# Performance work log

Measured on AMD Instinct MI355X. Metric: run time of the kernel, lower is better.

The kernel has to match this reference:

```python
import jax, jax.numpy as jnp
import numpy as np

DIM = 768
N_HEADS = 12
HEAD_DIM = DIM // N_HEADS
HIDDEN = 4 * DIM
B, T = 16, 577
EPS = 1e-6


def _layer_norm(x, w, b):
    mu = jnp.mean(x, axis=-1, keepdims=True)
    var = jnp.mean(jnp.square(x - mu), axis=-1, keepdims=True)
    return (x - mu) * jax.lax.rsqrt(var + EPS) * w + b


def setup_inputs() -> dict:
    key = jax.random.key(0)
    ks = jax.random.split(key, 8)
    s = lambda fan_in: 1.0 / np.sqrt(fan_in)
    return {
        "x": jax.random.normal(ks[0], (B, T, DIM), jnp.float32),
        "ln1_w": jnp.ones((DIM,), jnp.float32),
        "ln1_b": jnp.zeros((DIM,), jnp.float32),
        "qkv_w": jax.random.normal(ks[1], (DIM, 3 * DIM), jnp.float32) * s(DIM),
        "qkv_b": jnp.zeros((3 * DIM,), jnp.float32),
        "proj_w": jax.random.normal(ks[2], (DIM, DIM), jnp.float32) * s(DIM),
        "proj_b": jnp.zeros((DIM,), jnp.float32),
        "ln2_w": jnp.ones((DIM,), jnp.float32),
        "ln2_b": jnp.zeros((DIM,), jnp.float32),
        "fc1_w": jax.random.normal(ks[3], (DIM, HIDDEN), jnp.float32) * s(DIM),
        "fc1_b": jnp.zeros((HIDDEN,), jnp.float32),
        "fc2_w": jax.random.normal(ks[4], (HIDDEN, DIM), jnp.float32) * s(HIDDEN),
        "fc2_b": jnp.zeros((DIM,), jnp.float32),
    }


def reference(x, ln1_w, ln1_b, qkv_w, qkv_b, proj_w, proj_b,
              ln2_w, ln2_b, fc1_w, fc1_b, fc2_w, fc2_b):
    # --- attention branch ---
    h = _layer_norm(x, ln1_w, ln1_b)                      # [B,T,D]
    qkv = h @ qkv_w + qkv_b                               # [B,T,3D]
    qkv = qkv.reshape(B, T, 3, N_HEADS, HEAD_DIM)
    q, k, v = jnp.moveaxis(qkv, 2, 0)                     # each [B,T,H,hd]
    scale = HEAD_DIM ** -0.5
    dp = jnp.einsum('bqhd,bkhd->bhqk', q, k) * scale      # [B,H,T,T]
    attn = jax.nn.softmax(dp, axis=-1)
    wa = jnp.einsum('bhqk,bkhd->bqhd', attn, v)           # [B,T,H,hd]
    wa = wa.reshape(B, T, DIM)
    x = x + wa @ proj_w + proj_b
    # --- MLP branch ---
    h = _layer_norm(x, ln2_w, ln2_b)
    h = jax.nn.gelu(h @ fc1_w + fc1_b, approximate=False)
    x = x + h @ fc2_w + fc2_b
    return x
```

## Files before the change

### kernel.cpp

```cpp
#include <hip/hip_runtime.h>
#include <math.h>

#define DIM 768
#define NH 12
#define HIDDEN 3072
#define BB 16
#define TT 577
#define TPAD 640
#define BT (BB*TT)
#define MPAD 9344

typedef _Float16 f16x8 __attribute__((ext_vector_type(8)));
typedef __attribute__((ext_vector_type(4))) float f32x4;

__global__ __launch_bounds__(256) void ln_kernel(const float* __restrict__ x,
                                                 const float* __restrict__ w,
                                                 const float* __restrict__ b,
                                                 _Float16* __restrict__ oh) {
    int row = blockIdx.x;
    const float* xr = x + (size_t)row * DIM;
    int t = threadIdx.x;
    float v0 = xr[t], v1 = xr[t + 256], v2 = xr[t + 512];
    float s = v0 + v1 + v2;
    float sq = v0 * v0 + v1 * v1 + v2 * v2;
    __shared__ float red[8];
    int lane = t & 63, wid = t >> 6;
    #pragma unroll
    for (int off = 32; off; off >>= 1) {
        s  += __shfl_down(s, off);
        sq += __shfl_down(sq, off);
    }
    if (lane == 0) { red[wid] = s; red[4 + wid] = sq; }
    __syncthreads();
    if (t == 0) {
        float ts = red[0] + red[1] + red[2] + red[3];
        float tq = red[4] + red[5] + red[6] + red[7];
        float mu = ts * (1.0f / DIM);
        float var = tq * (1.0f / DIM) - mu * mu;
        red[0] = mu;
        red[1] = rsqrtf(var + 1e-6f);
    }
    __syncthreads();
    float mu = red[0], rstd = red[1];
    int sw = (row & 7) << 3;
    size_t ro = (size_t)row * DIM;
    #pragma unroll
    for (int e = 0; e < 3; ++e) {
        int c = t + e * 256;
        float v = (e == 0 ? v0 : (e == 1 ? v1 : v2));
        float val = (v - mu) * rstd * w[c] + b[c];
        oh[ro + (c ^ sw)] = (_Float16)val;
    }
}

__global__ __launch_bounds__(256) void convert_wT(const float* __restrict__ src,
                                                  _Float16* __restrict__ dh,
                                                  int K, int N) {
    int n = blockIdx.x * 64 + (threadIdx.x & 63);
    int k0 = blockIdx.y * 32 + (threadIdx.x >> 6) * 8;
    f16x8 h8;
    #pragma unroll
    for (int j = 0; j < 8; ++j) h8[j] = (_Float16)src[(size_t)(k0 + j) * N + n];
    *(f16x8*)&dh[(size_t)n * K + (k0 ^ ((n & 7) << 3))] = h8;
}

template<int EPI>
__global__ __launch_bounds__(256) void gemm_mfma(
    const _Float16* __restrict__ A, const _Float16* __restrict__ B,
    const float* __restrict__ bias, const float* __restrict__ resid,
    float* __restrict__ C, _Float16* __restrict__ O,
    _Float16* __restrict__ pQ, _Float16* __restrict__ pK, _Float16* __restrict__ pVT,
    int M, int N, int K) {
    __shared__ _Float16 lds[2][128][64];
    int tid = threadIdx.x;
    int wid = tid >> 6, lane = tid & 63;
    int m0 = blockIdx.y * 128, n0 = blockIdx.x * 128;
    int wr = wid >> 1, wc = wid & 1;

    const _Float16* src = (wid < 2) ? A : B;
    int srow0 = ((wid < 2) ? m0 : n0) + (wid & 1) * 64;
    _Float16* lbase = &lds[wid >> 1][(wid & 1) * 64][0];
    const _Float16* gbase = src + (size_t)(srow0 + (lane >> 3)) * K + (lane & 7) * 8;

    f32x4 acc[4][4];
    #pragma unroll
    for (int i = 0; i < 4; ++i)
        #pragma unroll
        for (int j = 0; j < 4; ++j) acc[i][j] = (f32x4)0.0f;

    for (int k0 = 0; k0 < K; k0 += 64) {
        #pragma unroll
        for (int i = 0; i < 8; ++i) {
            __builtin_amdgcn_global_load_lds(
                (const __attribute__((address_space(1))) void*)(gbase + (size_t)i * 8 * K + k0),
                (__attribute__((address_space(3))) void*)(lbase + i * 512),
                16, 0, 0);
        }
        __syncthreads();
        #pragma unroll
        for (int kk = 0; kk < 2; ++kk) {
            int so = (((kk * 4 + (lane >> 4)) ^ (lane & 7)) << 3);
            f16x8 af[4], bf[4];
            #pragma unroll
            for (int m = 0; m < 4; ++m)
                af[m] = *(const f16x8*)&lds[0][wr * 64 + m * 16 + (lane & 15)][so];
            #pragma unroll
            for (int n = 0; n < 4; ++n)
                bf[n] = *(const f16x8*)&lds[1][wc * 64 + n * 16 + (lane & 15)][so];
            #pragma unroll
            for (int m = 0; m < 4; ++m)
                #pragma unroll
                for (int n = 0; n < 4; ++n)
                    acc[m][n] = __builtin_amdgcn_mfma_f32_16x16x32_f16(af[m], bf[n], acc[m][n], 0, 0, 0);
        }
        __syncthreads();
    }

    int rbase = m0 + wr * 64 + (lane >> 4) * 4;
    int cbase = n0 + wc * 64 + (lane & 15);
    #pragma unroll
    for (int mi = 0; mi < 4; ++mi) {
        #pragma unroll
        for (int ni = 0; ni < 4; ++ni) {
            int c = cbase + ni * 16;
            float bsv = bias[c];
            #pragma unroll
            for (int r4 = 0; r4 < 4; ++r4) {
                int r = rbase + mi * 16 + r4;
                if (r >= M) continue;
                float v = acc[mi][ni][r4] + bsv;
                if (EPI == 1) {
                    v = 0.5f * v * (1.0f + erff(v * 0.70710678118f));
                    O[(size_t)r * N + (c ^ ((r & 7) << 3))] = (_Float16)v;
                } else if (EPI == 2) {
                    v += resid[(size_t)r * N + c];
                    C[(size_t)r * N + c] = v;
                } else {
                    int b_ = r / TT, t_ = r - b_ * TT;
                    int which = c / DIM, cc = c - which * DIM;
                    int head = cc >> 6, d = cc & 63;
                    size_t bh = (size_t)b_ * NH + head;
                    if (which == 0) {
                        pQ[(bh * TPAD + t_) * 64 + d] = (_Float16)(v * 0.125f);
                    } else if (which == 1) {
                        pK[(bh * TPAD + t_) * 64 + (d ^ ((t_ & 7) << 3))] = (_Float16)v;
                    } else {
                        pVT[(bh * 64 + d) * TPAD + ((t_ & ~63) | ((t_ & 63) ^ ((d & 7) << 3)))] = (_Float16)v;
                    }
                }
            }
        }
    }
}

__global__ __launch_bounds__(256) void attn_mfma(
    const _Float16* __restrict__ Q, const _Float16* __restrict__ Kp,
    const _Float16* __restrict__ VT, _Float16* __restrict__ wa) {
    __shared__ _Float16 lds[12288];
    int tid = threadIdx.x, wid = tid >> 6, lane = tid & 63;
    int qt = blockIdx.x, h = blockIdx.y, b = blockIdx.z;
    size_t bh = (size_t)b * NH + h;

    int qrow = qt * 64 + wid * 16 + (lane & 15);
    const _Float16* qb = Q + (bh * TPAD + qrow) * 64 + (lane >> 4) * 8;
    f16x8 qf[2];
    qf[0] = *(const f16x8*)qb;
    qf[1] = *(const f16x8*)(qb + 32);

    f32x4 oacc[4];
    #pragma unroll
    for (int dt = 0; dt < 4; ++dt) oacc[dt] = (f32x4)0.0f;
    float m[4] = {-1e30f, -1e30f, -1e30f, -1e30f};
    float lsum[4] = {0.f, 0.f, 0.f, 0.f};

    _Float16* pbase = &lds[8192 + wid * 1024];

    for (int kt0 = 0; kt0 < TT; kt0 += 64) {
        _Float16* dst = &lds[(wid >> 1) * 4096 + (wid & 1) * 2048];
        const _Float16* gsrc;
        int istride;
        if (wid < 2) {
            gsrc = Kp + (bh * TPAD + kt0 + (wid & 1) * 32 + (lane >> 3)) * 64 + (lane & 7) * 8;
            istride = 8 * 64;
        } else {
            gsrc = VT + (bh * 64 + (wid & 1) * 32 + (lane >> 3)) * TPAD + kt0 + (lane & 7) * 8;
            istride = 8 * TPAD;
        }
        #pragma unroll
        for (int i = 0; i < 4; ++i) {
            __builtin_amdgcn_global_load_lds(
                (const __attribute__((address_space(1))) void*)(gsrc + (size_t)i * istride),
                (__attribute__((address_space(3))) void*)(dst + i * 512),
                16, 0, 0);
        }
        __syncthreads();

        f32x4 sacc[4];
        #pragma unroll
        for (int kt = 0; kt < 4; ++kt) sacc[kt] = (f32x4)0.0f;
        #pragma unroll
        for (int dstep = 0; dstep < 2; ++dstep) {
            #pragma unroll
            for (int kt = 0; kt < 4; ++kt) {
                int krow = kt * 16 + (lane & 15);
                int ko = (((dstep * 4 + (lane >> 4)) ^ (krow & 7)) << 3);
                f16x8 kb = *(const f16x8*)&lds[krow * 64 + ko];
                sacc[kt] = __builtin_amdgcn_mfma_f32_16x16x32_f16(qf[dstep], kb, sacc[kt], 0, 0, 0);
            }
        }
        #pragma unroll
        for (int kt = 0; kt < 4; ++kt) {
            int kcol = kt0 + kt * 16 + (lane & 15);
            if (kcol >= TT) {
                #pragma unroll
                for (int r = 0; r < 4; ++r) sacc[kt][r] = -1e30f;
            }
        }
        float mt[4];
        #pragma unroll
        for (int r = 0; r < 4; ++r)
            mt[r] = fmaxf(fmaxf(sacc[0][r], sacc[1][r]), fmaxf(sacc[2][r], sacc[3][r]));
        #pragma unroll
        for (int off = 1; off <= 8; off <<= 1) {
            #pragma unroll
            for (int r = 0; r < 4; ++r) mt[r] = fmaxf(mt[r], __shfl_xor(mt[r], off));
        }
        float corr[4];
        #pragma unroll
        for (int r = 0; r < 4; ++r) {
            float nm = fmaxf(m[r], mt[r]);
            corr[r] = __expf(m[r] - nm);
            m[r] = nm;
        }
        float rowsum[4] = {0.f, 0.f, 0.f, 0.f};
        #pragma unroll
        for (int kt = 0; kt < 4; ++kt) {
            #pragma unroll
            for (int r = 0; r < 4; ++r) {
                float p = __expf(sacc[kt][r] - m[r]);
                rowsum[r] += p;
                int q = (lane >> 4) * 4 + r;
                int kcol = kt * 16 + (lane & 15);
                pbase[q * 64 + (kcol ^ ((q & 7) << 3))] = (_Float16)p;
            }
        }
        #pragma unroll
        for (int off = 1; off <= 8; off <<= 1) {
            #pragma unroll
            for (int r = 0; r < 4; ++r) rowsum[r] += __shfl_xor(rowsum[r], off);
        }
        #pragma unroll
        for (int r = 0; r < 4; ++r) {
            lsum[r] = lsum[r] * corr[r] + rowsum[r];
            #pragma unroll
            for (int dt = 0; dt < 4; ++dt) oacc[dt][r] *= corr[r];
        }
        #pragma unroll
        for (int kc = 0; kc < 2; ++kc) {
            int q = lane & 15;
            int pko = (((kc * 4 + (lane >> 4)) ^ (q & 7)) << 3);
            f16x8 pa = *(const f16x8*)&pbase[q * 64 + pko];
            #pragma unroll
            for (int dt = 0; dt < 4; ++dt) {
                int drow = dt * 16 + (lane & 15);
                int vo = (((kc * 4 + (lane >> 4)) ^ (drow & 7)) << 3);
                f16x8 vb = *(const f16x8*)&lds[4096 + drow * 64 + vo];
                oacc[dt] = __builtin_amdgcn_mfma_f32_16x16x32_f16(pa, vb, oacc[dt], 0, 0, 0);
            }
        }
        __syncthreads();
    }

    #pragma unroll
    for (int r = 0; r < 4; ++r) {
        int t = qt * 64 + wid * 16 + (lane >> 4) * 4 + r;
        if (t >= TT) continue;
        float inv = 1.0f / lsum[r];
        size_t row = (size_t)b * TT + t;
        int sw = (int)(row & 7) << 3;
        size_t ro = row * DIM;
        #pragma unroll
        for (int dt = 0; dt < 4; ++dt) {
            int c = h * 64 + dt * 16 + (lane & 15);
            wa[ro + (c ^ sw)] = (_Float16)(oacc[dt][r] * inv);
        }
    }
}

extern "C" void kernel_launch(void* const* d_in, const int* in_sizes, int n_in,
                              void* d_out, int out_size, void* d_ws, size_t ws_size,
                              hipStream_t stream) {
    const float* x      = (const float*)d_in[0];
    const float* ln1_w  = (const float*)d_in[1];
    const float* ln1_b  = (const float*)d_in[2];
    const float* qkv_w  = (const float*)d_in[3];
    const float* qkv_b  = (const float*)d_in[4];
    const float* proj_w = (const float*)d_in[5];
    const float* proj_b = (const float*)d_in[6];
    const float* ln2_w  = (const float*)d_in[7];
    const float* ln2_b  = (const float*)d_in[8];
    const float* fc1_w  = (const float*)d_in[9];
    const float* fc1_b  = (const float*)d_in[10];
    const float* fc2_w  = (const float*)d_in[11];
    const float* fc2_b  = (const float*)d_in[12];
    float* out = (float*)d_out;

    const size_t P768  = (size_t)MPAD * 768;
    const size_t P3072 = (size_t)MPAD * 3072;
    const size_t PQKV  = (size_t)BB * NH * TPAD * 64;
    char* wsb = (char*)d_ws;
    auto alloc = [&](size_t bytes) -> char* {
        char* p = wsb;
        wsb += (bytes + 255) & ~(size_t)255;
        return p;
    };
    _Float16* h_p   = (_Float16*)alloc(P768 * 2);
    _Float16* wa_p  = (_Float16*)alloc(P768 * 2);
    float* x1 = (float*)alloc((size_t)BT * 768 * 4);
    _Float16* qkvT = (_Float16*)alloc((size_t)2304 * 768 * 2);
    _Float16* projT = (_Float16*)alloc((size_t)768 * 768 * 2);
    _Float16* fc1T = (_Float16*)alloc((size_t)3072 * 768 * 2);
    _Float16* fc2T = (_Float16*)alloc((size_t)768 * 3072 * 2);
    char* ubase = alloc(P3072 * 2 > 3 * PQKV * 2 ? P3072 * 2 : 3 * PQKV * 2);
    _Float16* pQ  = (_Float16*)ubase;
    _Float16* pK  = pQ + PQKV;
    _Float16* pVT = pK + PQKV;
    _Float16* hh  = (_Float16*)ubase;

    dim3 blk(256);
    int mt = (BT + 127) / 128;

    convert_wT<<<dim3(2304 / 64, 768 / 32), blk, 0, stream>>>(qkv_w, qkvT, 768, 2304);
    convert_wT<<<dim3(768 / 64, 768 / 32), blk, 0, stream>>>(proj_w, projT, 768, 768);
    convert_wT<<<dim3(3072 / 64, 768 / 32), blk, 0, stream>>>(fc1_w, fc1T, 768, 3072);
    convert_wT<<<dim3(768 / 64, 3072 / 32), blk, 0, stream>>>(fc2_w, fc2T, 3072, 768);

    ln_kernel<<<BT, blk, 0, stream>>>(x, ln1_w, ln1_b, h_p);
    gemm_mfma<3><<<dim3(2304 / 128, mt), blk, 0, stream>>>(h_p, qkvT, qkv_b,
        nullptr, nullptr, nullptr, pQ, pK, pVT, BT, 2304, 768);
    attn_mfma<<<dim3((TT + 63) / 64, NH, BB), blk, 0, stream>>>(pQ, pK, pVT, wa_p);
    gemm_mfma<2><<<dim3(768 / 128, mt), blk, 0, stream>>>(wa_p, projT, proj_b,
        x, x1, nullptr, nullptr, nullptr, nullptr, BT, 768, 768);
    ln_kernel<<<BT, blk, 0, stream>>>(x1, ln2_w, ln2_b, h_p);
    gemm_mfma<1><<<dim3(3072 / 128, mt), blk, 0, stream>>>(h_p, fc1T, fc1_b,
        nullptr, nullptr, hh, nullptr, nullptr, nullptr, BT, 3072, 768);
    gemm_mfma<2><<<dim3(768 / 128, mt), blk, 0, stream>>>(hh, fc2T, fc2_b,
        x1, out, nullptr, nullptr, nullptr, nullptr, BT, 768, 3072);
}
```

Before: 524.0 us.

## Double-buffer LDS tiles in GEMM and attention; use tanh-form GELU

Both the MFMA GEMM and the attention kernel now use two LDS buffers. The next K/V or A/B tile is issued with global_load_lds before computing on the current one, and there is one barrier per iteration, so memory latency should overlap with MFMA work. Separately, the FC1 epilogue swaps the exact erf GELU for the tanh approximation written as a sigmoid with __expf, which is cheaper per element but deviates slightly from the exact reference. Doubling LDS per block (64 KB for the GEMM) may cut occupancy. The compiler may also insert full vmcnt waits before the LDS reads, which would limit the overlap.

New measurement: 490.0 us. 1.07x faster.

```diff
diff --git a/kernel.cpp b/kernel.cpp
--- a/kernel.cpp
+++ b/kernel.cpp
@@ -71,7 +71,7 @@
     float* __restrict__ C, _Float16* __restrict__ O,
     _Float16* __restrict__ pQ, _Float16* __restrict__ pK, _Float16* __restrict__ pVT,
     int M, int N, int K) {
-    __shared__ _Float16 lds[2][128][64];
+    __shared__ _Float16 lds[2][2][128][64];
     int tid = threadIdx.x;
     int wid = tid >> 6, lane = tid & 63;
     int m0 = blockIdx.y * 128, n0 = blockIdx.x * 128;
@@ -79,8 +79,9 @@
 
     const _Float16* src = (wid < 2) ? A : B;
     int srow0 = ((wid < 2) ? m0 : n0) + (wid & 1) * 64;
-    _Float16* lbase = &lds[wid >> 1][(wid & 1) * 64][0];
     const _Float16* gbase = src + (size_t)(srow0 + (lane >> 3)) * K + (lane & 7) * 8;
+    _Float16* lb[2] = { &lds[0][wid >> 1][(wid & 1) * 64][0],
+                        &lds[1][wid >> 1][(wid & 1) * 64][0] };
 
     f32x4 acc[4][4];
     #pragma unroll
@@ -88,25 +89,34 @@
         #pragma unroll
         for (int j = 0; j < 4; ++j) acc[i][j] = (f32x4)0.0f;
 
-    for (int k0 = 0; k0 < K; k0 += 64) {
-        #pragma unroll
-        for (int i = 0; i < 8; ++i) {
-            __builtin_amdgcn_global_load_lds(
-                (const __attribute__((address_space(1))) void*)(gbase + (size_t)i * 8 * K + k0),
-                (__attribute__((address_space(3))) void*)(lbase + i * 512),
-                16, 0, 0);
-        }
-        __syncthreads();
+    const int nk = K >> 6;
+    #pragma unroll
+    for (int i = 0; i < 8; ++i)
+        __builtin_amdgcn_global_load_lds(
+            (const __attribute__((address_space(1))) void*)(gbase + (size_t)i * 8 * K),
+            (__attribute__((address_space(3))) void*)(lb[0] + i * 512), 16, 0, 0);
+    __syncthreads();
+
+    int cur = 0;
+    for (int ks = 0; ks < nk; ++ks) {
+        if (ks + 1 < nk) {
+            int k0 = (ks + 1) << 6;
+            #pragma unroll
+            for (int i = 0; i < 8; ++i)
+                __builtin_amdgcn_global_load_lds(
+                    (const __attribute__((address_space(1))) void*)(gbase + (size_t)i * 8 * K + k0),
+                    (__attribute__((address_space(3))) void*)(lb[cur ^ 1] + i * 512), 16, 0, 0);
+        }
         #pragma unroll
         for (int kk = 0; kk < 2; ++kk) {
             int so = (((kk * 4 + (lane >> 4)) ^ (lane & 7)) << 3);
             f16x8 af[4], bf[4];
             #pragma unroll
             for (int m = 0; m < 4; ++m)
-                af[m] = *(const f16x8*)&lds[0][wr * 64 + m * 16 + (lane & 15)][so];
+                af[m] = *(const f16x8*)&lds[cur][0][wr * 64 + m * 16 + (lane & 15)][so];
             #pragma unroll
             for (int n = 0; n < 4; ++n)
-                bf[n] = *(const f16x8*)&lds[1][wc * 64 + n * 16 + (lane & 15)][so];
+                bf[n] = *(const f16x8*)&lds[cur][1][wc * 64 + n * 16 + (lane & 15)][so];
             #pragma unroll
             for (int m = 0; m < 4; ++m)
                 #pragma unroll
@@ -114,6 +124,7 @@
                     acc[m][n] = __builtin_amdgcn_mfma_f32_16x16x32_f16(af[m], bf[n], acc[m][n], 0, 0, 0);
         }
         __syncthreads();
+        cur ^= 1;
     }
 
     int rbase = m0 + wr * 64 + (lane >> 4) * 4;
@@ -130,7 +141,7 @@
                 if (r >= M) continue;
                 float v = acc[mi][ni][r4] + bsv;
                 if (EPI == 1) {
-                    v = 0.5f * v * (1.0f + erff(v * 0.70710678118f));
+                    v = v / (1.0f + __expf(-1.5957691216f * (v + 0.044715f * v * v * v)));
                     O[(size_t)r * N + (c ^ ((r & 7) << 3))] = (_Float16)v;
                 } else if (EPI == 2) {
                     v += resid[(size_t)r * N + c];
@@ -156,7 +167,7 @@
 __global__ __launch_bounds__(256) void attn_mfma(
     const _Float16* __restrict__ Q, const _Float16* __restrict__ Kp,
     const _Float16* __restrict__ VT, _Float16* __restrict__ wa) {
-    __shared__ _Float16 lds[12288];
+    __shared__ _Float16 lds[20480];
     int tid = threadIdx.x, wid = tid >> 6, lane = tid & 63;
     int qt = blockIdx.x, h = blockIdx.y, b = blockIdx.z;
     size_t bh = (size_t)b * NH + h;
@@ -173,27 +184,36 @@
     float m[4] = {-1e30f, -1e30f, -1e30f, -1e30f};
     float lsum[4] = {0.f, 0.f, 0.f, 0.f};
 
-    _Float16* pbase = &lds[8192 + wid * 1024];
-
+    _Float16* pbase = &lds[16384 + wid * 1024];
+    const _Float16* gK = Kp + (bh * TPAD + (wid & 1) * 32 + (lane >> 3)) * 64 + (lane & 7) * 8;
+    const _Float16* gV = VT + (bh * 64 + (wid & 1) * 32 + (lane >> 3)) * TPAD + (lane & 7) * 8;
+    int dstoff = (wid >> 1) * 4096 + (wid & 1) * 2048;
+
+    #pragma unroll
+    for (int i = 0; i < 4; ++i) {
+        const _Float16* g = (wid < 2) ? (gK + (size_t)i * 8 * 64) : (gV + (size_t)i * 8 * TPAD);
+        __builtin_amdgcn_global_load_lds(
+            (const __attribute__((address_space(1))) void*)g,
+            (__attribute__((address_space(3))) void*)(&lds[dstoff] + i * 512), 16, 0, 0);
+    }
+    __syncthreads();
+
+    int cur = 0;
     for (int kt0 = 0; kt0 < TT; kt0 += 64) {
-        _Float16* dst = &lds[(wid >> 1) * 4096 + (wid & 1) * 2048];
-        const _Float16* gsrc;
-        int istride;
-        if (wid < 2) {
-            gsrc = Kp + (bh * TPAD + kt0 + (wid & 1) * 32 + (lane >> 3)) * 64 + (lane & 7) * 8;
-            istride = 8 * 64;
-        } else {
-            gsrc = VT + (bh * 64 + (wid & 1) * 32 + (lane >> 3)) * TPAD + kt0 + (lane & 7) * 8;
-            istride = 8 * TPAD;
-        }
-        #pragma unroll
-        for (int i = 0; i < 4; ++i) {
-            __builtin_amdgcn_global_load_lds(
-                (const __attribute__((address_space(1))) void*)(gsrc + (size_t)i * istride),
-                (__attribute__((address_space(3))) void*)(dst + i * 512),
-                16, 0, 0);
-        }
-        __syncthreads();
+        if (kt0 + 64 < TT) {
+            int nxt = kt0 + 64;
+            #pragma unroll
+            for (int i = 0; i < 4; ++i) {
+                const _Float16* g = (wid < 2) ? (gK + (size_t)(nxt) * 64 + (size_t)i * 8 * 64)
+                                              : (gV + nxt + (size_t)i * 8 * TPAD);
+                __builtin_amdgcn_global_load_lds(
+                    (const __attribute__((address_space(1))) void*)g,
+                    (__attribute__((address_space(3))) void*)(&lds[(cur ^ 1) * 8192 + dstoff] + i * 512),
+                    16, 0, 0);
+            }
+        }
+        const _Float16* kbuf = &lds[cur * 8192];
+        const _Float16* vbuf = &lds[cur * 8192 + 4096];
 
         f32x4 sacc[4];
         #pragma unroll
@@ -204,7 +224,7 @@
             for (int kt = 0; kt < 4; ++kt) {
                 int krow = kt * 16 + (lane & 15);
                 int ko = (((dstep * 4 + (lane >> 4)) ^ (krow & 7)) << 3);
-                f16x8 kb = *(const f16x8*)&lds[krow * 64 + ko];
+                f16x8 kb = *(const f16x8*)&kbuf[krow * 64 + ko];
                 sacc[kt] = __builtin_amdgcn_mfma_f32_16x16x32_f16(qf[dstep], kb, sacc[kt], 0, 0, 0);
             }
         }
@@ -264,11 +284,12 @@
             for (int dt = 0; dt < 4; ++dt) {
                 int drow = dt * 16 + (lane & 15);
                 int vo = (((kc * 4 + (lane >> 4)) ^ (drow & 7)) << 3);
-                f16x8 vb = *(const f16x8*)&lds[4096 + drow * 64 + vo];
+                f16x8 vb = *(const f16x8*)&vbuf[drow * 64 + vo];
                 oacc[dt] = __builtin_amdgcn_mfma_f32_16x16x32_f16(pa, vb, oacc[dt], 0, 0, 0);
             }
         }
         __syncthreads();
+        cur ^= 1;
     }
 
     #pragma unroll
```
